# Kernel tuning notes

Hardware: AMD Instinct MI355X
Metric: run time of the kernel (lower is better)

## Reference

```python
import jax, jax.numpy as jnp
import numpy as np
import math

WS = (8, 8)        # window_size for context (2D)
HEADS = 8


def _attend(q, k, v, h):
    # q: (Bw, Nq, inner), k/v: (Bw, Nk, inner)
    Bw, Nq, inner = q.shape
    d = inner // h
    q = q.reshape(Bw, Nq, h, d)
    k = k.reshape(Bw, -1, h, d)
    v = v.reshape(Bw, -1, h, d)
    scores = jnp.einsum('bqhd,bkhd->bhqk', q, k) * (d ** -0.5)
    attn = jax.nn.softmax(scores, axis=-1)
    out = jnp.einsum('bhqk,bkhd->bqhd', attn, v)
    return out.reshape(Bw, Nq, inner)


def reference(x, context, W_q, W_k, W_v, W_out, b_out):
    B, C, T, H, W = x.shape
    H_, W_ = context.shape[-2], context.shape[-1]
    ws = WS
    assert H_ * W_ > ws[0] * ws[1] and H * W >= ws[0] * ws[1]  # window branch
    # pad context to multiple of window_size (no-op for chosen shapes)
    pad_r_2d = (-W_) % ws[1]
    pad_b_2d = (-H_) % ws[0]
    context = jnp.pad(context, ((0, 0), (0, 0), (0, pad_b_2d), (0, pad_r_2d)))
    # scaled window size for the (smaller) 3D query tensor
    ws_ = (math.ceil(float(ws[0]) * H / H_), math.ceil(float(ws[1]) * W / W_))
    pad_r_3d = (-W) % ws_[1]
    pad_b_3d = (-H) % ws_[0]
    x = jnp.pad(x, ((0, 0), (0, 0), (0, 0), (0, pad_b_3d), (0, pad_r_3d)))
    Hp, Wp = x.shape[-2], x.shape[-1]
    Hc, Wc = context.shape[-2], context.shape[-1]
    # window partition: context (B,C,Hc,Wc) -> (B*h*w, ws0*ws1, C)
    hc, wc = Hc // ws[0], Wc // ws[1]
    ctx = context.reshape(B, C, hc, ws[0], wc, ws[1])
    ctx = ctx.transpose(0, 2, 4, 3, 5, 1).reshape(B * hc * wc, ws[0] * ws[1], C)
    # window partition: x (B,C,T,Hp,Wp) -> (B*h*w, T*ws_0*ws_1, C)
    hg, wg = Hp // ws_[0], Wp // ws_[1]
    xw = x.reshape(B, C, T, hg, ws_[0], wg, ws_[1])
    xw = xw.transpose(0, 3, 5, 2, 4, 6, 1).reshape(B * hg * wg, T * ws_[0] * ws_[1], C)
    # QKV projections (no bias: qkv_bias=False, to_k always bias-free)
    q = xw @ W_q
    k = ctx @ W_k
    v = ctx @ W_v
    out = _attend(q, k, v, HEADS)  # (Bw, Nq, inner)
    inner = out.shape[-1]
    # window reverse -> (B, inner, T, Hp, Wp)
    out = out.reshape(B, hg, wg, T, ws_[0], ws_[1], inner)
    out = out.transpose(0, 6, 3, 1, 4, 2, 5).reshape(B, inner, T, Hp, Wp)
    out = out[:, :, :, :H, :W]
    # b c t h w -> b (t h w) c
    out = out.transpose(0, 2, 3, 4, 1).reshape(B, T * H * W, inner)
    return out @ W_out + b_out


def setup_inputs() -> dict:
    key = jax.random.key(0)
    ks = jax.random.split(key, 7)
    D = 512
    s = 0.02
    return {
        'x': jax.random.normal(ks[0], (4, D, 4, 32, 32), jnp.float32),
        'context': jax.random.normal(ks[1], (4, D, 128, 128), jnp.float32),
        'W_q': jax.random.normal(ks[2], (D, D), jnp.float32) * s,
        'W_k': jax.random.normal(ks[3], (D, D), jnp.float32) * s,
        'W_v': jax.random.normal(ks[4], (D, D), jnp.float32) * s,
        'W_out': jax.random.normal(ks[5], (D, D), jnp.float32) * s,
        'b_out': jnp.zeros((D,), jnp.float32),
    }
```

## Files before the change

### kernel.cpp

```cpp
#include <hip/hip_runtime.h>
#include <hip/hip_bf16.h>

typedef unsigned short u16;
typedef unsigned int u32;
typedef __attribute__((ext_vector_type(4))) float f32x4;
typedef __attribute__((ext_vector_type(4))) u16 u16x4;
typedef __attribute__((ext_vector_type(8))) u16 u16x8;
typedef __attribute__((ext_vector_type(8))) short s16x8;

__device__ __forceinline__ u16 f2bf(float f) {
    union { float f; u32 u; } v; v.f = f;
    u32 r = v.u + 0x7FFFu + ((v.u >> 16) & 1u);
    return (u16)(r >> 16);
}

__device__ __forceinline__ void gl_lds16(const u16* g, u16* l) {
    __builtin_amdgcn_global_load_lds(
        (const __attribute__((address_space(1))) unsigned int*)(const void*)g,
        (__attribute__((address_space(3))) unsigned int*)(void*)l, 16, 0, 0);
}

__global__ __launch_bounds__(256) void wtrans_kernel(
    const float* __restrict__ w0, const float* __restrict__ w1,
    const float* __restrict__ w2, const float* __restrict__ w3,
    u16* __restrict__ dst) {
    __shared__ float t[64][65];
    int wsel = blockIdx.x >> 6;
    int tile = blockIdx.x & 63;
    int j0 = (tile >> 3) * 64, c0 = (tile & 7) * 64;
    const float* src = wsel == 0 ? w0 : wsel == 1 ? w1 : wsel == 2 ? w2 : w3;
    u16* out = dst + (long)wsel * 512 * 512;
    int tj = threadIdx.x & 63;
    int ti = threadIdx.x >> 6;
#pragma unroll
    for (int p = 0; p < 16; ++p) {
        int row = p * 4 + ti;
        t[row][tj] = src[(long)(c0 + row) * 512 + j0 + tj];
    }
    __syncthreads();
#pragma unroll
    for (int p = 0; p < 16; ++p) {
        int jl = p * 4 + ti;
        out[(long)(j0 + jl) * 512 + c0 + tj] = f2bf(t[tj][jl]);
    }
}

__global__ __launch_bounds__(256) void permx_kernel(const float* __restrict__ x, u16* __restrict__ Aq) {
    __shared__ u16 t[64][36];
    int bid = blockIdx.x;
    int cb = bid & 7; bid >>= 3;
    int y  = bid & 31; bid >>= 5;
    int tt = bid & 3; bid >>= 2;
    int b  = bid;
    int tid = threadIdx.x;
    long ibase = ((long)(b * 512 + cb * 64) * 4 + tt) * 1024 + y * 32;
#pragma unroll
    for (int p = 0; p < 2; ++p) {
        int task = p * 256 + tid;
        int cc = task >> 3, xl = (task & 7) * 4;
        float4 v = *(const float4*)&x[ibase + (long)cc * 4096 + xl];
        u16x4 o = {f2bf(v.x), f2bf(v.y), f2bf(v.z), f2bf(v.w)};
        *(u16x4*)&t[cc][xl] = o;
    }
    __syncthreads();
    {
        int xx = tid >> 3, j = tid & 7;
        u16x8 o;
#pragma unroll
        for (int i = 0; i < 8; ++i) o[i] = t[j * 8 + i][xx];
        int row = b * 4096 + (y >> 1) * 256 + (xx >> 1) * 16 + tt * 4 + (y & 1) * 2 + (xx & 1);
        *(u16x8*)&Aq[(long)row * 512 + cb * 64 + j * 8] = o;
    }
}

__global__ __launch_bounds__(256) void permc_kernel(const float* __restrict__ ctx, u16* __restrict__ Actx) {
    __shared__ u16 t[64][68];
    int bid = blockIdx.x;
    int cb = bid & 7; bid >>= 3;
    int xb = bid & 1; bid >>= 1;
    int y  = bid & 127; bid >>= 7;
    int b  = bid;
    int tid = threadIdx.x;
    long ibase = ((long)(b * 512 + cb * 64) * 128 + y) * 128 + xb * 64;
#pragma unroll
    for (int p = 0; p < 4; ++p) {
        int task = p * 256 + tid;
        int cc = task >> 4, xl = (task & 15) * 4;
        float4 v = *(const float4*)&ctx[ibase + (long)cc * 16384 + xl];
        u16x4 o = {f2bf(v.x), f2bf(v.y), f2bf(v.z), f2bf(v.w)};
        *(u16x4*)&t[cc][xl] = o;
    }
    __syncthreads();
#pragma unroll
    for (int p = 0; p < 2; ++p) {
        int task = p * 256 + tid;
        int xx = task >> 3, j = task & 7;
        u16x8 o;
#pragma unroll
        for (int i = 0; i < 8; ++i) o[i] = t[j * 8 + i][xx];
        int xg = xb * 64 + xx;
        int row = b * 16384 + (y >> 3) * 1024 + (xg >> 3) * 64 + (y & 7) * 8 + (xg & 7);
        *(u16x8*)&Actx[(long)row * 512 + cb * 64 + j * 8] = o;
    }
}

template <int FINAL>
__global__ __launch_bounds__(256, 4) void gemm128_kernel(
    const u16* __restrict__ A, const u16* __restrict__ Bt,
    u16* __restrict__ Cb, float* __restrict__ Cf, const float* __restrict__ bias) {
    __shared__ u16 As[1024 * 8];
    __shared__ u16 Bs[1024 * 8];
    int tid = threadIdx.x;
    int lane = tid & 63;
    int w = tid >> 6;
    int wm = w >> 1, wn = w & 1;
    int bid = blockIdx.x;
    int wg = (bid & 7) * 64 + (bid >> 3);
    int m0 = (wg >> 2) * 128;
    int n0 = (wg & 3) * 128;

    const f32x4 z = {0.f, 0.f, 0.f, 0.f};
    f32x4 acc[4][4];
#pragma unroll
    for (int i = 0; i < 4; ++i)
#pragma unroll
        for (int j = 0; j < 4; ++j) acc[i][j] = z;

    int aoff[4], boff[4], lb[4];
#pragma unroll
    for (int i = 0; i < 4; ++i) {
        int s = i * 256 + tid;
        int row = s >> 3;
        int cb = (s & 7) ^ (row & 7);
        aoff[i] = (m0 + row) * 512 + cb * 8;
        boff[i] = (n0 + row) * 512 + cb * 8;
        lb[i] = (i * 256 + w * 64) * 8;
    }
    int la = lane & 15, lg = lane >> 4;
    for (int ks = 0; ks < 8; ++ks) {
        int ko = ks * 64;
#pragma unroll
        for (int i = 0; i < 4; ++i) {
            gl_lds16(&A[aoff[i] + ko], &As[lb[i]]);
            gl_lds16(&Bt[boff[i] + ko], &Bs[lb[i]]);
        }
        __syncthreads();
#pragma unroll
        for (int kk = 0; kk < 2; ++kk) {
            int cb = kk * 4 + lg;
            s16x8 af[4], bfr[4];
#pragma unroll
            for (int mt = 0; mt < 4; ++mt) {
                int r = wm * 64 + mt * 16 + la;
                af[mt] = *(const s16x8*)&As[r * 64 + ((cb ^ (r & 7)) * 8)];
            }
#pragma unroll
            for (int nt = 0; nt < 4; ++nt) {
                int c = wn * 64 + nt * 16 + la;
                bfr[nt] = *(const s16x8*)&Bs[c * 64 + ((cb ^ (c & 7)) * 8)];
            }
#pragma unroll
            for (int mt = 0; mt < 4; ++mt)
#pragma unroll
                for (int nt = 0; nt < 4; ++nt)
                    acc[mt][nt] = __builtin_amdgcn_mfma_f32_16x16x32_bf16(af[mt], bfr[nt], acc[mt][nt], 0, 0, 0);
        }
        __syncthreads();
    }
#pragma unroll
    for (int mt = 0; mt < 4; ++mt) {
#pragma unroll
        for (int nt = 0; nt < 4; ++nt) {
            int col = n0 + wn * 64 + nt * 16 + la;
#pragma unroll
            for (int rr = 0; rr < 4; ++rr) {
                int r = m0 + wm * 64 + mt * 16 + lg * 4 + rr;
                float v = acc[mt][nt][rr];
                if (FINAL) {
                    int bb = r >> 12, hg = (r >> 8) & 15, wgx = (r >> 4) & 15;
                    int tt = (r >> 2) & 3, rr0 = (r >> 1) & 1, cc0 = r & 1;
                    int tok = bb * 4096 + tt * 1024 + (hg * 2 + rr0) * 32 + wgx * 2 + cc0;
                    Cf[(long)tok * 512 + col] = v + bias[col];
                } else {
                    Cb[(long)r * 512 + col] = f2bf(v);
                }
            }
        }
    }
}

__global__ __launch_bounds__(512, 2) void gemmkv256_kernel(
    const u16* __restrict__ A, const u16* __restrict__ B, u16* __restrict__ C) {
    __shared__ u16 lds[2][2][16384];
    int tid = threadIdx.x;
    int lane = tid & 63;
    int w = tid >> 6;
    int wm = w >> 2, wn = w & 3;
    int la = lane & 15, lg = lane >> 4;
    int bid = blockIdx.x;
    int wg = (bid & 7) * 128 + (bid >> 3);
    int m0 = (wg >> 2) * 256;
    int n0 = (wg & 3) * 256;

    const f32x4 z = {0.f, 0.f, 0.f, 0.f};
    f32x4 acc[8][4];
#pragma unroll
    for (int i = 0; i < 8; ++i)
#pragma unroll
        for (int j = 0; j < 4; ++j) acc[i][j] = z;

    int aoff[4], boff[4], lsl[4];
#pragma unroll
    for (int i = 0; i < 4; ++i) {
        int s = i * 512 + tid;
        int row = s >> 3;
        int cb = (s & 7) ^ (row & 7);
        aoff[i] = (m0 + row) * 512 + cb * 8;
        boff[i] = (n0 + row) * 512 + cb * 8;
        lsl[i] = (i * 512 + w * 64) * 8;
    }

    s16x8 bfr[4][2];

#pragma unroll
    for (int i = 0; i < 4; ++i) {
        gl_lds16(&A[aoff[i]], &lds[0][0][lsl[i]]);
        gl_lds16(&B[boff[i]], &lds[0][1][lsl[i]]);
    }
#pragma unroll
    for (int i = 0; i < 4; ++i) {
        gl_lds16(&A[aoff[i] + 64], &lds[1][0][lsl[i]]);
        gl_lds16(&B[boff[i] + 64], &lds[1][1][lsl[i]]);
    }
    asm volatile("s_waitcnt vmcnt(8)" ::: "memory");
    __builtin_amdgcn_s_barrier();
    asm volatile("" ::: "memory");

#pragma unroll
    for (int t = 0; t < 8; ++t) {
        int buf = t & 1;
        const u16* Ab = lds[buf][0];
        const u16* Bb = lds[buf][1];
        int ko2 = (t + 2) * 64;

        {
            int cb = lg;
            s16x8 af[4];
#pragma unroll
            for (int mt = 0; mt < 4; ++mt) {
                int r = wm * 128 + mt * 16 + la;
                af[mt] = *(const s16x8*)&Ab[r * 64 + ((cb ^ (r & 7)) * 8)];
            }
#pragma unroll
            for (int nt = 0; nt < 4; ++nt) {
                int c = wn * 64 + nt * 16 + la;
                bfr[nt][0] = *(const s16x8*)&Bb[c * 64 + ((cb ^ (c & 7)) * 8)];
            }
            __builtin_amdgcn_s_barrier();
            __builtin_amdgcn_s_setprio(1);
#pragma unroll
            for (int mt = 0; mt < 4; ++mt)
#pragma unroll
                for (int nt = 0; nt < 4; ++nt)
                    acc[mt][nt] = __builtin_amdgcn_mfma_f32_16x16x32_bf16(af[mt], bfr[nt][0], acc[mt][nt], 0, 0, 0);
            __builtin_amdgcn_s_setprio(0);
            __builtin_amdgcn_sched_barrier(0);
            __builtin_amdgcn_s_barrier();
        }
        {
            int cb = 4 + lg;
            s16x8 af[4];
#pragma unroll
            for (int mt = 0; mt < 4; ++mt) {
                int r = wm * 128 + mt * 16 + la;
                af[mt] = *(const s16x8*)&Ab[r * 64 + ((cb ^ (r & 7)) * 8)];
            }
#pragma unroll
            for (int nt = 0; nt < 4; ++nt) {
                int c = wn * 64 + nt * 16 + la;
                bfr[nt][1] = *(const s16x8*)&Bb[c * 64 + ((cb ^ (c & 7)) * 8)];
            }
            __builtin_amdgcn_s_barrier();
            __builtin_amdgcn_s_setprio(1);
#pragma unroll
            for (int mt = 0; mt < 4; ++mt)
#pragma unroll
                for (int nt = 0; nt < 4; ++nt)
                    acc[mt][nt] = __builtin_amdgcn_mfma_f32_16x16x32_bf16(af[mt], bfr[nt][1], acc[mt][nt], 0, 0, 0);
            __builtin_amdgcn_s_setprio(0);
            __builtin_amdgcn_sched_barrier(0);
            __builtin_amdgcn_s_barrier();
        }
        {
            int cb = 4 + lg;
            s16x8 af[4];
#pragma unroll
            for (int mt = 0; mt < 4; ++mt) {
                int r = wm * 128 + 64 + mt * 16 + la;
                af[mt] = *(const s16x8*)&Ab[r * 64 + ((cb ^ (r & 7)) * 8)];
            }
            if (t < 6) {
                gl_lds16(&B[boff[0] + ko2], &lds[buf][1][lsl[0]]);
                gl_lds16(&B[boff[1] + ko2], &lds[buf][1][lsl[1]]);
                gl_lds16(&A[aoff[0] + ko2], &lds[buf][0][lsl[0]]);
            }
            __builtin_amdgcn_s_barrier();
            __builtin_amdgcn_s_setprio(1);
#pragma unroll
            for (int mt = 0; mt < 4; ++mt)
#pragma unroll
                for (int nt = 0; nt < 4; ++nt)
                    acc[4 + mt][nt] = __builtin_amdgcn_mfma_f32_16x16x32_bf16(af[mt], bfr[nt][1], acc[4 + mt][nt], 0, 0, 0);
            __builtin_amdgcn_s_setprio(0);
            __builtin_amdgcn_sched_barrier(0);
            __builtin_amdgcn_s_barrier();
        }
        {
            int cb = lg;
            s16x8 af[4];
#pragma unroll
            for (int mt = 0; mt < 4; ++mt) {
                int r = wm * 128 + 64 + mt * 16 + la;
                af[mt] = *(const s16x8*)&Ab[r * 64 + ((cb ^ (r & 7)) * 8)];
            }
            if (t < 6) {
                gl_lds16(&B[boff[2] + ko2], &lds[buf][1][lsl[2]]);
                gl_lds16(&B[boff[3] + ko2], &lds[buf][1][lsl[3]]);
                gl_lds16(&A[aoff[2] + ko2], &lds[buf][0][lsl[2]]);
            }
            __builtin_amdgcn_s_barrier();
            __builtin_amdgcn_s_setprio(1);
#pragma unroll
            for (int mt = 0; mt < 4; ++mt)
#pragma unroll
                for (int nt = 0; nt < 4; ++nt)
                    acc[4 + mt][nt] = __builtin_amdgcn_mfma_f32_16x16x32_bf16(af[mt], bfr[nt][0], acc[4 + mt][nt], 0, 0, 0);
            __builtin_amdgcn_s_setprio(0);
            __builtin_amdgcn_sched_barrier(0);
            __builtin_amdgcn_s_barrier();
        }
        if (t < 6) {
            gl_lds16(&A[aoff[1] + ko2], &lds[buf][0][lsl[1]]);
            gl_lds16(&A[aoff[3] + ko2], &lds[buf][0][lsl[3]]);
            asm volatile("s_waitcnt vmcnt(8)" ::: "memory");
            __builtin_amdgcn_s_barrier();
            asm volatile("" ::: "memory");
        } else if (t == 6) {
            asm volatile("s_waitcnt vmcnt(0)" ::: "memory");
            __builtin_amdgcn_s_barrier();
            asm volatile("" ::: "memory");
        }
    }

#pragma unroll
    for (int mt = 0; mt < 8; ++mt) {
#pragma unroll
        for (int nt = 0; nt < 4; ++nt) {
            int col = n0 + wn * 64 + nt * 16 + la;
#pragma unroll
            for (int rr = 0; rr < 4; ++rr) {
                int r = m0 + wm * 128 + mt * 16 + lg * 4 + rr;
                C[(long)r * 1024 + col] = f2bf(acc[mt][nt][rr]);
            }
        }
    }
}

__global__ __launch_bounds__(64) void attn_kernel(
    const u16* __restrict__ Q, const u16* __restrict__ KV, u16* __restrict__ O) {
    __shared__ u16 P[16 * 104];
    int bid = blockIdx.x;
    int wg = (bid & 7) * 1024 + (bid >> 3);
    int win = wg >> 3;
    int h = wg & 7;
    int lane = threadIdx.x;
    int la = lane & 15, lg = lane >> 4;
    const u16* Qb = Q + (long)win * 16 * 512 + h * 64;
    const u16* Kb = KV + (long)win * 64 * 1024 + h * 64;
    const u16* Vb = KV + (long)win * 64 * 1024 + 512 + h * 64;

    s16x8 qf[2];
#pragma unroll
    for (int kk = 0; kk < 2; ++kk)
        qf[kk] = *(const s16x8*)&Qb[la * 512 + kk * 32 + lg * 8];

    const f32x4 z = {0.f, 0.f, 0.f, 0.f};
    f32x4 st[4];
#pragma unroll
    for (int rt = 0; rt < 4; ++rt) st[rt] = z;
#pragma unroll
    for (int rt = 0; rt < 4; ++rt)
#pragma unroll
        for (int kk = 0; kk < 2; ++kk) {
            s16x8 kf = *(const s16x8*)&Kb[(rt * 16 + la) * 1024 + kk * 32 + lg * 8];
            st[rt] = __builtin_amdgcn_mfma_f32_16x16x32_bf16(kf, qf[kk], st[rt], 0, 0, 0);
        }
    float mloc = -1e30f;
#pragma unroll
    for (int rt = 0; rt < 4; ++rt)
#pragma unroll
        for (int rr = 0; rr < 4; ++rr) {
            st[rt][rr] *= 0.125f;
            mloc = fmaxf(mloc, st[rt][rr]);
        }
    mloc = fmaxf(mloc, __shfl_xor(mloc, 16));
    mloc = fmaxf(mloc, __shfl_xor(mloc, 32));
    float p[4][4];
    float sloc = 0.f;
#pragma unroll
    for (int rt = 0; rt < 4; ++rt)
#pragma unroll
        for (int rr = 0; rr < 4; ++rr) {
            p[rt][rr] = __expf(st[rt][rr] - mloc);
            sloc += p[rt][rr];
        }
    sloc += __shfl_xor(sloc, 16);
    sloc += __shfl_xor(sloc, 32);
    float inv = 1.0f / sloc;
#pragma unroll
    for (int rt = 0; rt < 4; ++rt)
#pragma unroll
        for (int rr = 0; rr < 4; ++rr)
            P[la * 104 + rt * 16 + lg * 4 + rr] = f2bf(p[rt][rr] * inv);
    __syncthreads();

    f32x4 od[4];
#pragma unroll
    for (int dt = 0; dt < 4; ++dt) od[dt] = z;
#pragma unroll
    for (int kk2 = 0; kk2 < 2; ++kk2) {
        s16x8 pa = *(const s16x8*)&P[la * 104 + kk2 * 32 + lg * 8];
#pragma unroll
        for (int dt = 0; dt < 4; ++dt) {
            s16x8 vb;
#pragma unroll
            for (int j = 0; j < 8; ++j)
                vb[j] = (short)Vb[(long)(kk2 * 32 + lg * 8 + j) * 1024 + dt * 16 + la];
            od[dt] = __builtin_amdgcn_mfma_f32_16x16x32_bf16(pa, vb, od[dt], 0, 0, 0);
        }
    }
    u16* Ob = O + (long)win * 16 * 512 + h * 64;
#pragma unroll
    for (int dt = 0; dt < 4; ++dt)
#pragma unroll
        for (int rr = 0; rr < 4; ++rr)
            Ob[(long)(lg * 4 + rr) * 512 + dt * 16 + la] = f2bf(od[dt][rr]);
}

__global__ void sentinel_kernel(float* out) {
    if (threadIdx.x == 0 && blockIdx.x == 0) out[0] = -12345.0f;
}

extern "C" void kernel_launch(void* const* d_in, const int* in_sizes, int n_in,
                              void* d_out, int out_size, void* d_ws, size_t ws_size,
                              hipStream_t stream) {
    const float* x   = (const float*)d_in[0];
    const float* ctx = (const float*)d_in[1];
    const float* Wq  = (const float*)d_in[2];
    const float* Wk  = (const float*)d_in[3];
    const float* Wv  = (const float*)d_in[4];
    const float* Wo  = (const float*)d_in[5];
    const float* bo  = (const float*)d_in[6];
    float* out = (float*)d_out;

    u16* wsb  = (u16*)d_ws;
    u16* WT   = wsb;
    u16* Aq   = WT + 4l * 262144;
    u16* Actx = Aq + 8388608l;
    u16* Qb   = Actx + 33554432l;
    u16* KVb  = Qb + 8388608l;
    u16* Ob   = KVb + 67108864l;
    size_t need = (size_t)(126877696l) * 2;
    if (ws_size < need) {
        sentinel_kernel<<<1, 64, 0, stream>>>(out);
        return;
    }

    wtrans_kernel<<<256, 256, 0, stream>>>(Wq, Wk, Wv, Wo, WT);
    permx_kernel<<<4096, 256, 0, stream>>>(x, Aq);
    permc_kernel<<<8192, 256, 0, stream>>>(ctx, Actx);
    gemm128_kernel<0><<<512, 256, 0, stream>>>(Aq, WT, Qb, nullptr, nullptr);
    gemmkv256_kernel<<<1024, 512, 0, stream>>>(Actx, WT + 262144l, KVb);
    attn_kernel<<<8192, 64, 0, stream>>>(Qb, KVb, Ob);
    gemm128_kernel<1><<<512, 256, 0, stream>>>(Ob, WT + 3l * 262144, nullptr, out, bo);
}
```

Baseline: 203.1 us.

## Merge prep kernels into one launch and store V transposed per window

Folds the three preprocessing kernels (weight transpose, x permute, context permute) into a single launch with a block-index switch, which removes two kernel launches and their tails. The KV GEMM epilogue now writes K and V to separate buffers, with V stored transposed per window and head. The attention kernel can then load V fragments with one 16-byte vector load instead of eight strided scalar loads. The transposed V store scatters 8-byte writes, which may cost some write efficiency in the GEMM epilogue.

```diff
diff --git a/kernel.cpp b/kernel.cpp
--- a/kernel.cpp
+++ b/kernel.cpp
@@ -7,6 +7,7 @@
 typedef __attribute__((ext_vector_type(4))) u16 u16x4;
 typedef __attribute__((ext_vector_type(8))) u16 u16x8;
 typedef __attribute__((ext_vector_type(8))) short s16x8;
+typedef __attribute__((ext_vector_type(2))) u32 u32x2;
 
 __device__ __forceinline__ u16 f2bf(float f) {
     union { float f; u32 u; } v; v.f = f;
@@ -20,87 +21,88 @@
         (__attribute__((address_space(3))) unsigned int*)(void*)l, 16, 0, 0);
 }
 
-__global__ __launch_bounds__(256) void wtrans_kernel(
+__global__ __launch_bounds__(256) void prep_kernel(
     const float* __restrict__ w0, const float* __restrict__ w1,
-    const float* __restrict__ w2, const float* __restrict__ w3,
-    u16* __restrict__ dst) {
-    __shared__ float t[64][65];
-    int wsel = blockIdx.x >> 6;
-    int tile = blockIdx.x & 63;
-    int j0 = (tile >> 3) * 64, c0 = (tile & 7) * 64;
-    const float* src = wsel == 0 ? w0 : wsel == 1 ? w1 : wsel == 2 ? w2 : w3;
-    u16* out = dst + (long)wsel * 512 * 512;
-    int tj = threadIdx.x & 63;
-    int ti = threadIdx.x >> 6;
-#pragma unroll
-    for (int p = 0; p < 16; ++p) {
-        int row = p * 4 + ti;
-        t[row][tj] = src[(long)(c0 + row) * 512 + j0 + tj];
-    }
-    __syncthreads();
-#pragma unroll
-    for (int p = 0; p < 16; ++p) {
-        int jl = p * 4 + ti;
-        out[(long)(j0 + jl) * 512 + c0 + tj] = f2bf(t[tj][jl]);
-    }
-}
-
-__global__ __launch_bounds__(256) void permx_kernel(const float* __restrict__ x, u16* __restrict__ Aq) {
-    __shared__ u16 t[64][36];
+    const float* __restrict__ w2, const float* __restrict__ w3, u16* __restrict__ WT,
+    const float* __restrict__ x, u16* __restrict__ Aq,
+    const float* __restrict__ ctx, u16* __restrict__ Actx) {
+    __shared__ char smem[16640];
     int bid = blockIdx.x;
-    int cb = bid & 7; bid >>= 3;
-    int y  = bid & 31; bid >>= 5;
-    int tt = bid & 3; bid >>= 2;
-    int b  = bid;
     int tid = threadIdx.x;
-    long ibase = ((long)(b * 512 + cb * 64) * 4 + tt) * 1024 + y * 32;
-#pragma unroll
-    for (int p = 0; p < 2; ++p) {
-        int task = p * 256 + tid;
-        int cc = task >> 3, xl = (task & 7) * 4;
-        float4 v = *(const float4*)&x[ibase + (long)cc * 4096 + xl];
-        u16x4 o = {f2bf(v.x), f2bf(v.y), f2bf(v.z), f2bf(v.w)};
-        *(u16x4*)&t[cc][xl] = o;
-    }
-    __syncthreads();
-    {
-        int xx = tid >> 3, j = tid & 7;
-        u16x8 o;
-#pragma unroll
-        for (int i = 0; i < 8; ++i) o[i] = t[j * 8 + i][xx];
-        int row = b * 4096 + (y >> 1) * 256 + (xx >> 1) * 16 + tt * 4 + (y & 1) * 2 + (xx & 1);
-        *(u16x8*)&Aq[(long)row * 512 + cb * 64 + j * 8] = o;
-    }
-}
-
-__global__ __launch_bounds__(256) void permc_kernel(const float* __restrict__ ctx, u16* __restrict__ Actx) {
-    __shared__ u16 t[64][68];
-    int bid = blockIdx.x;
-    int cb = bid & 7; bid >>= 3;
-    int xb = bid & 1; bid >>= 1;
-    int y  = bid & 127; bid >>= 7;
-    int b  = bid;
-    int tid = threadIdx.x;
-    long ibase = ((long)(b * 512 + cb * 64) * 128 + y) * 128 + xb * 64;
-#pragma unroll
-    for (int p = 0; p < 4; ++p) {
-        int task = p * 256 + tid;
-        int cc = task >> 4, xl = (task & 15) * 4;
-        float4 v = *(const float4*)&ctx[ibase + (long)cc * 16384 + xl];
-        u16x4 o = {f2bf(v.x), f2bf(v.y), f2bf(v.z), f2bf(v.w)};
-        *(u16x4*)&t[cc][xl] = o;
-    }
-    __syncthreads();
-#pragma unroll
-    for (int p = 0; p < 2; ++p) {
-        int task = p * 256 + tid;
-        int xx = task >> 3, j = task & 7;
-        u16x8 o;
-#pragma unroll
-        for (int i = 0; i < 8; ++i) o[i] = t[j * 8 + i][xx];
-        int xg = xb * 64 + xx;
-        int row = b * 16384 + (y >> 3) * 1024 + (xg >> 3) * 64 + (y & 7) * 8 + (xg & 7);
-        *(u16x8*)&Actx[(long)row * 512 + cb * 64 + j * 8] = o;
+    if (bid < 8192) {
+        u16 (*t)[68] = (u16(*)[68])smem;
+        int b2 = bid;
+        int cb = b2 & 7; b2 >>= 3;
+        int xb = b2 & 1; b2 >>= 1;
+        int y  = b2 & 127; b2 >>= 7;
+        int b  = b2;
+        long ibase = ((long)(b * 512 + cb * 64) * 128 + y) * 128 + xb * 64;
+#pragma unroll
+        for (int p = 0; p < 4; ++p) {
+            int task = p * 256 + tid;
+            int cc = task >> 4, xl = (task & 15) * 4;
+            float4 v = *(const float4*)&ctx[ibase + (long)cc * 16384 + xl];
+            u16x4 o = {f2bf(v.x), f2bf(v.y), f2bf(v.z), f2bf(v.w)};
+            *(u16x4*)&t[cc][xl] = o;
+        }
+        __syncthreads();
+#pragma unroll
+        for (int p = 0; p < 2; ++p) {
+            int task = p * 256 + tid;
+            int xx = task >> 3, j = task & 7;
+            u16x8 o;
+#pragma unroll
+            for (int i = 0; i < 8; ++i) o[i] = t[j * 8 + i][xx];
+            int xg = xb * 64 + xx;
+            int row = b * 16384 + (y >> 3) * 1024 + (xg >> 3) * 64 + (y & 7) * 8 + (xg & 7);
+            *(u16x8*)&Actx[(long)row * 512 + cb * 64 + j * 8] = o;
+        }
+    } else if (bid < 12288) {
+        u16 (*t)[36] = (u16(*)[36])smem;
+        int b2 = bid - 8192;
+        int cb = b2 & 7; b2 >>= 3;
+        int y  = b2 & 31; b2 >>= 5;
+        int tt = b2 & 3; b2 >>= 2;
+        int b  = b2;
+        long ibase = ((long)(b * 512 + cb * 64) * 4 + tt) * 1024 + y * 32;
+#pragma unroll
+        for (int p = 0; p < 2; ++p) {
+            int task = p * 256 + tid;
+            int cc = task >> 3, xl = (task & 7) * 4;
+            float4 v = *(const float4*)&x[ibase + (long)cc * 4096 + xl];
+            u16x4 o = {f2bf(v.x), f2bf(v.y), f2bf(v.z), f2bf(v.w)};
+            *(u16x4*)&t[cc][xl] = o;
+        }
+        __syncthreads();
+        {
+            int xx = tid >> 3, j = tid & 7;
+            u16x8 o;
+#pragma unroll
+            for (int i = 0; i < 8; ++i) o[i] = t[j * 8 + i][xx];
+            int row = b * 4096 + (y >> 1) * 256 + (xx >> 1) * 16 + tt * 4 + (y & 1) * 2 + (xx & 1);
+            *(u16x8*)&Aq[(long)row * 512 + cb * 64 + j * 8] = o;
+        }
+    } else {
+        float (*t)[65] = (float(*)[65])smem;
+        int b2 = bid - 12288;
+        int wsel = b2 >> 6;
+        int tile = b2 & 63;
+        int j0 = (tile >> 3) * 64, c0 = (tile & 7) * 64;
+        const float* src = wsel == 0 ? w0 : wsel == 1 ? w1 : wsel == 2 ? w2 : w3;
+        u16* out = WT + (long)wsel * 512 * 512;
+        int tj = tid & 63;
+        int ti = tid >> 6;
+#pragma unroll
+        for (int p = 0; p < 16; ++p) {
+            int row = p * 4 + ti;
+            t[row][tj] = src[(long)(c0 + row) * 512 + j0 + tj];
+        }
+        __syncthreads();
+#pragma unroll
+        for (int p = 0; p < 16; ++p) {
+            int jl = p * 4 + ti;
+            out[(long)(j0 + jl) * 512 + c0 + tj] = f2bf(t[tj][jl]);
+        }
     }
 }
 
@@ -190,7 +192,8 @@
 }
 
 __global__ __launch_bounds__(512, 2) void gemmkv256_kernel(
-    const u16* __restrict__ A, const u16* __restrict__ B, u16* __restrict__ C) {
+    const u16* __restrict__ A, const u16* __restrict__ B,
+    u16* __restrict__ CK, u16* __restrict__ CVT) {
     __shared__ u16 lds[2][2][16384];
     int tid = threadIdx.x;
     int lane = tid & 63;
@@ -352,22 +355,41 @@
         }
     }
 
-#pragma unroll
-    for (int mt = 0; mt < 8; ++mt) {
-#pragma unroll
-        for (int nt = 0; nt < 4; ++nt) {
-            int col = n0 + wn * 64 + nt * 16 + la;
-#pragma unroll
-            for (int rr = 0; rr < 4; ++rr) {
-                int r = m0 + wm * 128 + mt * 16 + lg * 4 + rr;
-                C[(long)r * 1024 + col] = f2bf(acc[mt][nt][rr]);
+    if ((wg & 3) < 2) {
+#pragma unroll
+        for (int mt = 0; mt < 8; ++mt) {
+#pragma unroll
+            for (int nt = 0; nt < 4; ++nt) {
+                int col = n0 + wn * 64 + nt * 16 + la;
+#pragma unroll
+                for (int rr = 0; rr < 4; ++rr) {
+                    int r = m0 + wm * 128 + mt * 16 + lg * 4 + rr;
+                    CK[(long)r * 512 + col] = f2bf(acc[mt][nt][rr]);
+                }
+            }
+        }
+    } else {
+        int colb = n0 - 512 + wn * 64;
+        int winb = (m0 >> 6) + wm * 2;
+#pragma unroll
+        for (int mt = 0; mt < 8; ++mt) {
+            int win = winb + (mt >> 2);
+            int kvr = (mt & 3) * 16 + lg * 4;
+#pragma unroll
+            for (int nt = 0; nt < 4; ++nt) {
+                int colp = colb + nt * 16 + la;
+                u32 lo = (u32)f2bf(acc[mt][nt][0]) | ((u32)f2bf(acc[mt][nt][1]) << 16);
+                u32 hi = (u32)f2bf(acc[mt][nt][2]) | ((u32)f2bf(acc[mt][nt][3]) << 16);
+                u32x2 pk = {lo, hi};
+                *(u32x2*)&CVT[(long)win * 32768 + colp * 64 + kvr] = pk;
             }
         }
     }
 }
 
 __global__ __launch_bounds__(64) void attn_kernel(
-    const u16* __restrict__ Q, const u16* __restrict__ KV, u16* __restrict__ O) {
+    const u16* __restrict__ Q, const u16* __restrict__ K,
+    const u16* __restrict__ VT, u16* __restrict__ O) {
     __shared__ u16 P[16 * 104];
     int bid = blockIdx.x;
     int wg = (bid & 7) * 1024 + (bid >> 3);
@@ -376,8 +398,8 @@
     int lane = threadIdx.x;
     int la = lane & 15, lg = lane >> 4;
     const u16* Qb = Q + (long)win * 16 * 512 + h * 64;
-    const u16* Kb = KV + (long)win * 64 * 1024 + h * 64;
-    const u16* Vb = KV + (long)win * 64 * 1024 + 512 + h * 64;
+    const u16* Kb = K + (long)win * 64 * 512 + h * 64;
+    const u16* Vt = VT + (long)win * 32768 + h * 64 * 64;
 
     s16x8 qf[2];
 #pragma unroll
@@ -392,7 +414,7 @@
     for (int rt = 0; rt < 4; ++rt)
 #pragma unroll
         for (int kk = 0; kk < 2; ++kk) {
-            s16x8 kf = *(const s16x8*)&Kb[(rt * 16 + la) * 1024 + kk * 32 + lg * 8];
+            s16x8 kf = *(const s16x8*)&Kb[(rt * 16 + la) * 512 + kk * 32 + lg * 8];
             st[rt] = __builtin_amdgcn_mfma_f32_16x16x32_bf16(kf, qf[kk], st[rt], 0, 0, 0);
         }
     float mloc = -1e30f;
@@ -432,10 +454,7 @@
         s16x8 pa = *(const s16x8*)&P[la * 104 + kk2 * 32 + lg * 8];
 #pragma unroll
         for (int dt = 0; dt < 4; ++dt) {
-            s16x8 vb;
-#pragma unroll
-            for (int j = 0; j < 8; ++j)
-                vb[j] = (short)Vb[(long)(kk2 * 32 + lg * 8 + j) * 1024 + dt * 16 + la];
+            s16x8 vb = *(const s16x8*)&Vt[(dt * 16 + la) * 64 + kk2 * 32 + lg * 8];
             od[dt] = __builtin_amdgcn_mfma_f32_16x16x32_bf16(pa, vb, od[dt], 0, 0, 0);
         }
     }
@@ -468,19 +487,18 @@
     u16* Aq   = WT + 4l * 262144;
     u16* Actx = Aq + 8388608l;
     u16* Qb   = Actx + 33554432l;
-    u16* KVb  = Qb + 8388608l;
-    u16* Ob   = KVb + 67108864l;
+    u16* Kb   = Qb + 8388608l;
+    u16* VTb  = Kb + 33554432l;
+    u16* Ob   = VTb + 33554432l;
     size_t need = (size_t)(126877696l) * 2;
     if (ws_size < need) {
         sentinel_kernel<<<1, 64, 0, stream>>>(out);
         return;
     }
 
-    wtrans_kernel<<<256, 256, 0, stream>>>(Wq, Wk, Wv, Wo, WT);
-    permx_kernel<<<4096, 256, 0, stream>>>(x, Aq);
-    permc_kernel<<<8192, 256, 0, stream>>>(ctx, Actx);
+    prep_kernel<<<12544, 256, 0, stream>>>(Wq, Wk, Wv, Wo, WT, x, Aq, ctx, Actx);
     gemm128_kernel<0><<<512, 256, 0, stream>>>(Aq, WT, Qb, nullptr, nullptr);
-    gemmkv256_kernel<<<1024, 512, 0, stream>>>(Actx, WT + 262144l, KVb);
-    attn_kernel<<<8192, 64, 0, stream>>>(Qb, KVb, Ob);
+    gemmkv256_kernel<<<1024, 512, 0, stream>>>(Actx, WT + 262144l, Kb, VTb);
+    attn_kernel<<<8192, 64, 0, stream>>>(Qb, Kb, VTb, Ob);
     gemm128_kernel<1><<<512, 256, 0, stream>>>(Ob, WT + 3l * 262144, nullptr, out, bo);
 }
```

New measurement: 209.9 us. 1.03x slower.
